# Kernel tuning notes

Measured on AMD Instinct MI355X. Metric: run time of the kernel, lower is better.

The kernel has to match this reference:

```python
import jax, jax.numpy as jnp
import numpy as np

# Dimensions (match input_specs / init_kwargs)
B, T, M, H, E, K = 4, 2048, 1024, 2048, 8, 2
CAP_FACTOR = 1.0  # tutel default capacity_factor
S = B * T
C = int(K * CAP_FACTOR * ((S + E - 1) // E))  # per-expert capacity (tutel Top-k gate)


def setup_inputs() -> dict:
    key = jax.random.key(0)
    ks = jax.random.split(key, 4)
    x = jax.random.normal(ks[0], (B, T, M), jnp.float32)
    wg = jax.random.normal(ks[1], (M, E), jnp.float32) / np.sqrt(M)
    w1 = jax.random.normal(ks[2], (E, M, H), jnp.float32) / np.sqrt(M)
    b1 = jnp.zeros((E, H), jnp.float32)
    w2 = jax.random.normal(ks[3], (E, H, M), jnp.float32) / np.sqrt(H)
    b2 = jnp.zeros((E, M), jnp.float32)
    return {"x": x, "wg": wg, "w1": w1, "b1": b1, "w2": w2, "b2": b2}


def reference(x, wg, w1, b1, w2, b2):
    xf = x.reshape(S, M)
    # ---- Top-k gate (fp32 gate) ----
    logits = xf.astype(jnp.float32) @ wg                 # [S, E]
    scores = jax.nn.softmax(logits, axis=-1)
    topv, topi = jax.lax.top_k(scores, K)                # [S, K]
    gates = topv / (jnp.sum(topv, axis=-1, keepdims=True) + 1e-9)  # normalized top-k gates

    # ---- Dispatch into [E, C, M] buffer with capacity-based token dropping ----
    buf = jnp.zeros((E, C, M), xf.dtype)
    offset = jnp.zeros((E,), jnp.int32)  # tokens already placed per expert (previous slots)
    pos_list, keep_list = [], []
    for j in range(K):  # small fixed loop over top-k slots
        e = topi[:, j]                                   # [S]
        m = jax.nn.one_hot(e, E, dtype=jnp.int32)        # [S, E]
        pos = jnp.sum(jnp.cumsum(m, axis=0) * m, axis=1) - 1 + offset[e]  # position within expert
        offset = offset + jnp.sum(m, axis=0)
        keep = pos < C                                   # drop tokens over capacity
        posc = jnp.minimum(pos, C - 1)
        buf = buf.at[e, posc].add(xf * keep[:, None].astype(xf.dtype))
        pos_list.append(posc)
        keep_list.append(keep)

    # ---- Grouped expert FFN: relu(x W1 + b1) W2 + b2 ----
    h = jax.nn.relu(jnp.einsum('ecm,emh->ech', buf, w1) + b1[:, None, :])  # [E, C, H]
    y = jnp.einsum('ech,ehm->ecm', h, w2) + b2[:, None, :]                 # [E, C, M]

    # ---- Combine with gate weights ----
    out = jnp.zeros_like(xf)
    for j in range(K):
        g = gates[:, j] * keep_list[j].astype(xf.dtype)
        out = out + g[:, None] * y[topi[:, j], pos_list[j]]

    out = out.reshape(B, T, M)
    # result = log_softmax(sum over model_dim, over token dim)
    return jax.nn.log_softmax(jnp.sum(out, axis=2), axis=1)   # [B, T]
```

## Files before the change

kernel.cpp:

```cpp
#include <hip/hip_runtime.h>
#include <hip/hip_bf16.h>
#include <cstdint>
#include <cstddef>

constexpr int Bb = 4;
constexpr int Tt = 2048;
constexpr int Mm = 1024;
constexpr int Hh = 2048;
constexpr int Ee = 8;
constexpr int Ss = Bb * Tt;
constexpr int Cc = 2048;

typedef __attribute__((ext_vector_type(4))) float f32x4;
typedef __attribute__((ext_vector_type(8))) short bf16x8;

__device__ inline void load_lds16(const void* g, void* l) {
    __builtin_amdgcn_global_load_lds(
        (const __attribute__((address_space(1))) unsigned int*)g,
        (__attribute__((address_space(3))) unsigned int*)l, 16, 0, 0);
}

__global__ __launch_bounds__(256) void k_prep(
    const float* __restrict__ w1, const float* __restrict__ w2, const float* __restrict__ b2,
    const float* __restrict__ x, const float* __restrict__ wg,
    __hip_bfloat16* __restrict__ w1t, float* __restrict__ w2sum, float* __restrict__ b2sum,
    int* __restrict__ esel, float* __restrict__ gates, __hip_bfloat16* __restrict__ xbf) {
    int bid = blockIdx.x;
    int t = threadIdx.x;
    if (bid < 4096) {
        __shared__ float tile[64][65];
        int e = bid >> 9, m0 = ((bid >> 5) & 15) * 64, h0 = (bid & 31) * 64;
        const float* src = w1 + (size_t)e * Mm * Hh;
        #pragma unroll
        for (int i = 0; i < 4; i++) {
            int idx = t + i * 256;
            int r = idx >> 4, c4 = idx & 15;
            float4 v = *(const float4*)(src + (size_t)(m0 + r) * Hh + h0 + c4 * 4);
            tile[r][c4 * 4 + 0] = v.x; tile[r][c4 * 4 + 1] = v.y;
            tile[r][c4 * 4 + 2] = v.z; tile[r][c4 * 4 + 3] = v.w;
        }
        __syncthreads();
        __hip_bfloat16* dst = w1t + (size_t)e * Hh * Mm;
        #pragma unroll
        for (int i = 0; i < 2; i++) {
            int idx = t + i * 256;
            int r = idx >> 3, c8 = idx & 7;
            __hip_bfloat16 tmp[8];
            #pragma unroll
            for (int k = 0; k < 8; k++) tmp[k] = __float2bfloat16(tile[c8 * 8 + k][r]);
            uint4 vv; __builtin_memcpy(&vv, tmp, 16);
            *(uint4*)(dst + (size_t)(h0 + r) * Mm + m0 + c8 * 8) = vv;
        }
    } else if (bid < 8192) {
        int wave = t >> 6, lane = t & 63;
        int r = (bid - 4096) * 4 + wave;
        const float4* p = (const float4*)(w2 + (size_t)r * Mm);
        float s = 0.f;
        #pragma unroll
        for (int i = 0; i < 4; i++) { float4 v = p[lane + i * 64]; s += v.x + v.y + v.z + v.w; }
        #pragma unroll
        for (int off = 32; off; off >>= 1) s += __shfl_down(s, off);
        if (lane == 0) w2sum[r] = s;
    } else if (bid == 8192) {
        int wave = t >> 6, lane = t & 63;
        int e = wave * 2 + (lane >> 5);
        int l = lane & 31;
        const float4* p = (const float4*)(b2 + (size_t)e * Mm);
        float s = 0.f;
        #pragma unroll
        for (int i = 0; i < 8; i++) { float4 v = p[l + i * 32]; s += v.x + v.y + v.z + v.w; }
        #pragma unroll
        for (int off = 16; off; off >>= 1) s += __shfl_down(s, off);
        if (l == 0) b2sum[e] = s;
    } else {
        int gb = bid - 8193;
        int s = (gb * 256 + t) >> 6;
        int lane = t & 63;
        const float4* xr = (const float4*)(x + (size_t)s * Mm);
        const float4* wgr = (const float4*)wg;
        float acc[8];
        #pragma unroll
        for (int e = 0; e < 8; e++) acc[e] = 0.f;
        #pragma unroll
        for (int i = 0; i < 4; i++) {
            float4 xv = xr[lane + i * 64];
            __hip_bfloat16 tb[4];
            tb[0] = __float2bfloat16(xv.x); tb[1] = __float2bfloat16(xv.y);
            tb[2] = __float2bfloat16(xv.z); tb[3] = __float2bfloat16(xv.w);
            uint2 u; __builtin_memcpy(&u, tb, 8);
            *(uint2*)(xbf + (size_t)s * Mm + (lane + i * 64) * 4) = u;
            int mbase = (lane + i * 64) * 4;
            #pragma unroll
            for (int k = 0; k < 4; k++) {
                int m = mbase + k;
                float xm = (k == 0) ? xv.x : (k == 1) ? xv.y : (k == 2) ? xv.z : xv.w;
                float4 w0 = wgr[m * 2], w1v = wgr[m * 2 + 1];
                acc[0] += xm * w0.x;  acc[1] += xm * w0.y;  acc[2] += xm * w0.z;  acc[3] += xm * w0.w;
                acc[4] += xm * w1v.x; acc[5] += xm * w1v.y; acc[6] += xm * w1v.z; acc[7] += xm * w1v.w;
            }
        }
        #pragma unroll
        for (int off = 32; off; off >>= 1)
            #pragma unroll
            for (int e = 0; e < 8; e++) acc[e] += __shfl_down(acc[e], off);
        if (lane == 0) {
            float mx = acc[0];
            #pragma unroll
            for (int e = 1; e < 8; e++) mx = fmaxf(mx, acc[e]);
            float p[8], se = 0.f;
            #pragma unroll
            for (int e = 0; e < 8; e++) { p[e] = expf(acc[e] - mx); se += p[e]; }
            float inv = 1.f / se;
            #pragma unroll
            for (int e = 0; e < 8; e++) p[e] *= inv;
            int i0 = 0; float v0 = p[0];
            #pragma unroll
            for (int e = 1; e < 8; e++) if (p[e] > v0) { v0 = p[e]; i0 = e; }
            int i1 = -1; float v1 = -1.f;
            #pragma unroll
            for (int e = 0; e < 8; e++) if (e != i0 && p[e] > v1) { v1 = p[e]; i1 = e; }
            float den = v0 + v1 + 1e-9f;
            esel[s] = i0; esel[Ss + s] = i1;
            gates[s] = v0 / den; gates[Ss + s] = v1 / den;
        }
    }
}

__global__ __launch_bounds__(256) void k_posA(const int* __restrict__ esel,
                                              int* __restrict__ lrank, int* __restrict__ blockhist) {
    int b = blockIdx.x, t = threadIdx.x;
    int d = b * 256 + t;
    int e = esel[d];
    int wave = t >> 6, lane = t & 63;
    __shared__ int wh[4][8];
    unsigned long long mymask = 0;
    #pragma unroll
    for (int q = 0; q < 8; q++) {
        unsigned long long m = __ballot(e == q);
        if (q == e) mymask = m;
        if (lane == 0) wh[wave][q] = (int)__popcll(m);
    }
    __syncthreads();
    int prefix = (int)__popcll(mymask & ((1ull << lane) - 1ull));
    for (int w = 0; w < wave; w++) prefix += wh[w][e];
    lrank[d] = prefix;
    if (t < 8) blockhist[b * 8 + t] = wh[0][t] + wh[1][t] + wh[2][t] + wh[3][t];
}

__global__ __launch_bounds__(512) void k_posB(const int* __restrict__ blockhist,
                                              int* __restrict__ blockbase) {
    int t = threadIdx.x;
    int wave = t >> 6, lane = t & 63;
    int v = blockhist[lane * 8 + wave];
    int x = v;
    #pragma unroll
    for (int off = 1; off < 64; off <<= 1) {
        int y = __shfl_up(x, off);
        if (lane >= off) x += y;
    }
    blockbase[lane * 8 + wave] = x - v;
}

__global__ __launch_bounds__(256) void k_sidx(const int* __restrict__ esel,
                                              const int* __restrict__ lrank,
                                              const int* __restrict__ blockbase,
                                              int* __restrict__ pos, int* __restrict__ srcidx) {
    int d = blockIdx.x * 256 + threadIdx.x;
    int e = esel[d];
    int p = blockbase[(d >> 8) * 8 + e] + lrank[d];
    pos[d] = p;
    if (p < Cc) srcidx[e * Cc + p] = d & (Ss - 1);
}

__global__ __launch_bounds__(256) void k_gemm(
    const __hip_bfloat16* __restrict__ xbf, const int* __restrict__ srcidx,
    const __hip_bfloat16* __restrict__ w1t,
    const float* __restrict__ b1, const float* __restrict__ w2sum,
    float* __restrict__ rowsum) {
    __shared__ __align__(16) __hip_bfloat16 As[2][128 * 32];
    __shared__ __align__(16) __hip_bfloat16 Bs[2][128 * 32];
    int bid = blockIdx.x;
    int e = bid & 7;
    int tile = bid >> 3;
    int sq = tile >> 4, in16 = tile & 15;
    int hb = (sq & 3) * 4 + (in16 & 3);
    int cb = (sq >> 2) * 4 + (in16 >> 2);
    int c0 = cb * 128, h0 = hb * 128;
    int t = threadIdx.x;
    int wave = t >> 6, lane = t & 63;
    int wm = wave >> 1, wn = wave & 1;
    int r16 = lane & 15, quad = lane >> 4;
    int r_s = t >> 2;
    int qd = ((t & 3) - ((t >> 3) & 3)) & 3;
    int s0 = srcidx[e * Cc + c0 + r_s];
    int s1 = srcidx[e * Cc + c0 + 64 + r_s];
    const __hip_bfloat16* a0 = xbf + (size_t)s0 * Mm + qd * 8;
    const __hip_bfloat16* a1 = xbf + (size_t)s1 * Mm + qd * 8;
    const __hip_bfloat16* Bp = w1t + (size_t)e * Hh * Mm;
    const __hip_bfloat16* b0 = Bp + (size_t)(h0 + r_s) * Mm + qd * 8;
    const __hip_bfloat16* b1p = Bp + (size_t)(h0 + 64 + r_s) * Mm + qd * 8;
    int frag = r16 * 4 + ((quad + (r16 >> 1)) & 3);
    f32x4 acc[4][4];
    #pragma unroll
    for (int i = 0; i < 4; i++)
        #pragma unroll
        for (int j = 0; j < 4; j++) acc[i][j] = (f32x4){0.f, 0.f, 0.f, 0.f};

    load_lds16(a0,  As[0] + t * 8);
    load_lds16(a1,  As[0] + (256 + t) * 8);
    load_lds16(b0,  Bs[0] + t * 8);
    load_lds16(b1p, Bs[0] + (256 + t) * 8);

    #pragma unroll 2
    for (int tt = 0; tt < 32; ++tt) {
        int cur = tt & 1;
        __builtin_amdgcn_sched_barrier(0);
        if (tt < 31) {
            int k0 = (tt + 1) * 32;
            load_lds16(a0 + k0,  As[cur ^ 1] + t * 8);
            load_lds16(a1 + k0,  As[cur ^ 1] + (256 + t) * 8);
            load_lds16(b0 + k0,  Bs[cur ^ 1] + t * 8);
            load_lds16(b1p + k0, Bs[cur ^ 1] + (256 + t) * 8);
            asm volatile("s_waitcnt vmcnt(4)" ::: "memory");
        } else {
            asm volatile("s_waitcnt vmcnt(0)" ::: "memory");
        }
        __builtin_amdgcn_s_barrier();
        __builtin_amdgcn_sched_barrier(0);
        bf16x8 af[4], bfr[4];
        #pragma unroll
        for (int mi = 0; mi < 4; mi++)
            af[mi] = *(const bf16x8*)(As[cur] + (((wm * 4 + mi) * 64 + frag) * 8));
        #pragma unroll
        for (int ni = 0; ni < 4; ni++)
            bfr[ni] = *(const bf16x8*)(Bs[cur] + (((wn * 4 + ni) * 64 + frag) * 8));
        #pragma unroll
        for (int mi = 0; mi < 4; mi++)
            #pragma unroll
            for (int ni = 0; ni < 4; ni++)
                acc[mi][ni] = __builtin_amdgcn_mfma_f32_16x16x32_bf16(af[mi], bfr[ni], acc[mi][ni], 0, 0, 0);
        __builtin_amdgcn_sched_barrier(0);
        __builtin_amdgcn_s_barrier();
    }

    float b1v[4], wsv[4];
    #pragma unroll
    for (int ni = 0; ni < 4; ni++) {
        int hg = h0 + wn * 64 + ni * 16 + r16;
        b1v[ni] = b1[e * Hh + hg];
        wsv[ni] = w2sum[e * Hh + hg];
    }
    #pragma unroll
    for (int mi = 0; mi < 4; mi++) {
        #pragma unroll
        for (int r = 0; r < 4; r++) {
            float val = 0.f;
            #pragma unroll
            for (int ni = 0; ni < 4; ni++) {
                float sv = acc[mi][ni][r] + b1v[ni];
                val += fmaxf(sv, 0.f) * wsv[ni];
            }
            #pragma unroll
            for (int off = 1; off < 16; off <<= 1) val += __shfl_xor(val, off);
            if (r16 == 0) {
                int cg = c0 + wm * 64 + mi * 16 + quad * 4 + r;
                atomicAdd(&rowsum[e * Cc + cg], val);
            }
        }
    }
}

__global__ __launch_bounds__(256) void k_combine(
    const int* __restrict__ esel, const int* __restrict__ pos,
    const float* __restrict__ gates, const float* __restrict__ rowsum,
    const float* __restrict__ b2sum, float* __restrict__ vals) {
    int s = blockIdx.x * 256 + threadIdx.x;
    float acc = 0.f;
    #pragma unroll
    for (int j = 0; j < 2; j++) {
        int d = j * Ss + s;
        int p = pos[d];
        if (p < Cc) {
            int ee = esel[d];
            acc += gates[d] * (rowsum[ee * Cc + p] + b2sum[ee]);
        }
    }
    vals[s] = acc;
}

__global__ __launch_bounds__(1024) void k_lsm(const float* __restrict__ vals,
                                              float* __restrict__ out) {
    int b = blockIdx.x; int t = threadIdx.x;
    __shared__ float red[1024];
    float v0 = vals[b * Tt + t];
    float v1 = vals[b * Tt + t + 1024];
    float m = fmaxf(v0, v1);
    red[t] = m; __syncthreads();
    for (int st = 512; st; st >>= 1) { if (t < st) red[t] = fmaxf(red[t], red[t + st]); __syncthreads(); }
    float mx = red[0];
    __syncthreads();
    float se = expf(v0 - mx) + expf(v1 - mx);
    red[t] = se; __syncthreads();
    for (int st = 512; st; st >>= 1) { if (t < st) red[t] += red[t + st]; __syncthreads(); }
    float lse = logf(red[0]);
    out[b * Tt + t] = v0 - mx - lse;
    out[b * Tt + t + 1024] = v1 - mx - lse;
}

extern "C" void kernel_launch(void* const* d_in, const int* in_sizes, int n_in,
                              void* d_out, int out_size, void* d_ws, size_t ws_size,
                              hipStream_t stream) {
    const float* x  = (const float*)d_in[0];
    const float* wg = (const float*)d_in[1];
    const float* w1 = (const float*)d_in[2];
    const float* b1 = (const float*)d_in[3];
    const float* w2 = (const float*)d_in[4];
    const float* b2 = (const float*)d_in[5];
    float* out = (float*)d_out;

    char* ws = (char*)d_ws;
    size_t off = 0;
    auto alloc = [&](size_t bytes) -> void* {
        void* p = ws + off;
        off += (bytes + 255) & ~(size_t)255;
        return p;
    };
    float* rowsum   = (float*)alloc((size_t)Ee * Cc * 4 + (size_t)Ee * Cc * 4);
    int*   srcidx   = (int*)(rowsum + (size_t)Ee * Cc);
    float* w2sum    = (float*)alloc((size_t)Ee * Hh * 4);
    float* b2sum    = (float*)alloc(Ee * 4);
    int*   esel     = (int*)alloc((size_t)2 * Ss * 4);
    int*   lrank    = (int*)alloc((size_t)2 * Ss * 4);
    int*   blockhist= (int*)alloc((size_t)64 * 8 * 4);
    int*   blockbase= (int*)alloc((size_t)64 * 8 * 4);
    int*   pos      = (int*)alloc((size_t)2 * Ss * 4);
    float* gates    = (float*)alloc((size_t)2 * Ss * 4);
    __hip_bfloat16* xbf = (__hip_bfloat16*)alloc((size_t)Ss * Mm * 2);
    __hip_bfloat16* w1t = (__hip_bfloat16*)alloc((size_t)Ee * Hh * Mm * 2);

    hipMemsetAsync(rowsum, 0, (size_t)2 * Ee * Cc * 4, stream);
    k_prep<<<10241, 256, 0, stream>>>(w1, w2, b2, x, wg, w1t, w2sum, b2sum, esel, gates, xbf);
    k_posA<<<64, 256, 0, stream>>>(esel, lrank, blockhist);
    k_posB<<<1, 512, 0, stream>>>(blockhist, blockbase);
    k_sidx<<<64, 256, 0, stream>>>(esel, lrank, blockbase, pos, srcidx);
    k_gemm<<<2048, 256, 0, stream>>>(xbf, srcidx, w1t, b1, w2sum, rowsum);
    float* vals = (float*)lrank;
    k_combine<<<32, 256, 0, stream>>>(esel, pos, gates, rowsum, b2sum, vals);
    k_lsm<<<Bb, 1024, 0, stream>>>(vals, out);
}
```

Before: 308.5 us.

## Enlarge expert GEMM tiles to 256x256 with 8 waves and 4-stage LDS pipeline

```diff
diff --git a/kernel.cpp b/kernel.cpp
--- a/kernel.cpp
+++ b/kernel.cpp
@@ -172,76 +172,102 @@
     if (p < Cc) srcidx[e * Cc + p] = d & (Ss - 1);
 }
 
-__global__ __launch_bounds__(256) void k_gemm(
+__global__ __launch_bounds__(512, 2) void k_gemm(
     const __hip_bfloat16* __restrict__ xbf, const int* __restrict__ srcidx,
     const __hip_bfloat16* __restrict__ w1t,
     const float* __restrict__ b1, const float* __restrict__ w2sum,
     float* __restrict__ rowsum) {
-    __shared__ __align__(16) __hip_bfloat16 As[2][128 * 32];
-    __shared__ __align__(16) __hip_bfloat16 Bs[2][128 * 32];
+    __shared__ __align__(16) __hip_bfloat16 As[4][256 * 32];
+    __shared__ __align__(16) __hip_bfloat16 Bs[4][256 * 32];
     int bid = blockIdx.x;
     int e = bid & 7;
     int tile = bid >> 3;
-    int sq = tile >> 4, in16 = tile & 15;
-    int hb = (sq & 3) * 4 + (in16 & 3);
-    int cb = (sq >> 2) * 4 + (in16 >> 2);
-    int c0 = cb * 128, h0 = hb * 128;
+    int cb = tile >> 3, hb = tile & 7;
+    int c0 = cb * 256, h0 = hb * 256;
     int t = threadIdx.x;
     int wave = t >> 6, lane = t & 63;
-    int wm = wave >> 1, wn = wave & 1;
+    int wm = wave >> 2;
+    int wn = wave & 3;
     int r16 = lane & 15, quad = lane >> 4;
     int r_s = t >> 2;
     int qd = ((t & 3) - ((t >> 3) & 3)) & 3;
     int s0 = srcidx[e * Cc + c0 + r_s];
-    int s1 = srcidx[e * Cc + c0 + 64 + r_s];
+    int s1 = srcidx[e * Cc + c0 + 128 + r_s];
     const __hip_bfloat16* a0 = xbf + (size_t)s0 * Mm + qd * 8;
     const __hip_bfloat16* a1 = xbf + (size_t)s1 * Mm + qd * 8;
     const __hip_bfloat16* Bp = w1t + (size_t)e * Hh * Mm;
     const __hip_bfloat16* b0 = Bp + (size_t)(h0 + r_s) * Mm + qd * 8;
-    const __hip_bfloat16* b1p = Bp + (size_t)(h0 + 64 + r_s) * Mm + qd * 8;
-    int frag = r16 * 4 + ((quad + (r16 >> 1)) & 3);
-    f32x4 acc[4][4];
-    #pragma unroll
-    for (int i = 0; i < 4; i++)
+    const __hip_bfloat16* b1p = Bp + (size_t)(h0 + 128 + r_s) * Mm + qd * 8;
+    int fo = r16 * 4 + ((quad + (r16 >> 1)) & 3);
+    f32x4 acc[8][4];
+    #pragma unroll
+    for (int i = 0; i < 8; i++)
         #pragma unroll
         for (int j = 0; j < 4; j++) acc[i][j] = (f32x4){0.f, 0.f, 0.f, 0.f};
 
-    load_lds16(a0,  As[0] + t * 8);
-    load_lds16(a1,  As[0] + (256 + t) * 8);
-    load_lds16(b0,  Bs[0] + t * 8);
-    load_lds16(b1p, Bs[0] + (256 + t) * 8);
-
-    #pragma unroll 2
-    for (int tt = 0; tt < 32; ++tt) {
-        int cur = tt & 1;
+    #pragma unroll
+    for (int p = 0; p < 3; p++) {
+        int k0 = p * 32;
+        load_lds16(a0 + k0,  As[p] + t * 8);
+        load_lds16(a1 + k0,  As[p] + (512 + t) * 8);
+        load_lds16(b0 + k0,  Bs[p] + t * 8);
+        load_lds16(b1p + k0, Bs[p] + (512 + t) * 8);
+    }
+
+    for (int j = 0; j < 29; ++j) {
         __builtin_amdgcn_sched_barrier(0);
-        if (tt < 31) {
-            int k0 = (tt + 1) * 32;
-            load_lds16(a0 + k0,  As[cur ^ 1] + t * 8);
-            load_lds16(a1 + k0,  As[cur ^ 1] + (256 + t) * 8);
-            load_lds16(b0 + k0,  Bs[cur ^ 1] + t * 8);
-            load_lds16(b1p + k0, Bs[cur ^ 1] + (256 + t) * 8);
-            asm volatile("s_waitcnt vmcnt(4)" ::: "memory");
-        } else {
-            asm volatile("s_waitcnt vmcnt(0)" ::: "memory");
-        }
+        asm volatile("s_waitcnt vmcnt(8)" ::: "memory");
         __builtin_amdgcn_s_barrier();
         __builtin_amdgcn_sched_barrier(0);
-        bf16x8 af[4], bfr[4];
-        #pragma unroll
-        for (int mi = 0; mi < 4; mi++)
-            af[mi] = *(const bf16x8*)(As[cur] + (((wm * 4 + mi) * 64 + frag) * 8));
+        {
+            int b = (j + 3) & 3;
+            int k0 = (j + 3) * 32;
+            load_lds16(a0 + k0,  As[b] + t * 8);
+            load_lds16(a1 + k0,  As[b] + (512 + t) * 8);
+            load_lds16(b0 + k0,  Bs[b] + t * 8);
+            load_lds16(b1p + k0, Bs[b] + (512 + t) * 8);
+        }
+        const __hip_bfloat16* Ar = As[j & 3];
+        const __hip_bfloat16* Br = Bs[j & 3];
+        bf16x8 bfr[4];
         #pragma unroll
         for (int ni = 0; ni < 4; ni++)
-            bfr[ni] = *(const bf16x8*)(Bs[cur] + (((wn * 4 + ni) * 64 + frag) * 8));
-        #pragma unroll
-        for (int mi = 0; mi < 4; mi++)
+            bfr[ni] = *(const bf16x8*)(Br + ((wn * 4 + ni) * 64 + fo) * 8);
+        __builtin_amdgcn_s_setprio(1);
+        #pragma unroll
+        for (int mi = 0; mi < 8; mi++) {
+            bf16x8 af = *(const bf16x8*)(Ar + ((wm * 8 + mi) * 64 + fo) * 8);
             #pragma unroll
             for (int ni = 0; ni < 4; ni++)
-                acc[mi][ni] = __builtin_amdgcn_mfma_f32_16x16x32_bf16(af[mi], bfr[ni], acc[mi][ni], 0, 0, 0);
+                acc[mi][ni] = __builtin_amdgcn_mfma_f32_16x16x32_bf16(af, bfr[ni], acc[mi][ni], 0, 0, 0);
+        }
+        __builtin_amdgcn_s_setprio(0);
+    }
+    #pragma unroll
+    for (int j = 29; j < 32; ++j) {
         __builtin_amdgcn_sched_barrier(0);
+        if (j == 29)      asm volatile("s_waitcnt vmcnt(8)" ::: "memory");
+        else if (j == 30) asm volatile("s_waitcnt vmcnt(4)" ::: "memory");
+        else              asm volatile("s_waitcnt vmcnt(0)" ::: "memory");
         __builtin_amdgcn_s_barrier();
-    }
+        __builtin_amdgcn_sched_barrier(0);
+        const __hip_bfloat16* Ar = As[j & 3];
+        const __hip_bfloat16* Br = Bs[j & 3];
+        bf16x8 bfr[4];
+        #pragma unroll
+        for (int ni = 0; ni < 4; ni++)
+            bfr[ni] = *(const bf16x8*)(Br + ((wn * 4 + ni) * 64 + fo) * 8);
+        __builtin_amdgcn_s_setprio(1);
+        #pragma unroll
+        for (int mi = 0; mi < 8; mi++) {
+            bf16x8 af = *(const bf16x8*)(Ar + ((wm * 8 + mi) * 64 + fo) * 8);
+            #pragma unroll
+            for (int ni = 0; ni < 4; ni++)
+                acc[mi][ni] = __builtin_amdgcn_mfma_f32_16x16x32_bf16(af, bfr[ni], acc[mi][ni], 0, 0, 0);
+        }
+        __builtin_amdgcn_s_setprio(0);
+    }
+    __builtin_amdgcn_sched_barrier(0);
 
     float b1v[4], wsv[4];
     #pragma unroll
@@ -251,7 +277,7 @@
         wsv[ni] = w2sum[e * Hh + hg];
     }
     #pragma unroll
-    for (int mi = 0; mi < 4; mi++) {
+    for (int mi = 0; mi < 8; mi++) {
         #pragma unroll
         for (int r = 0; r < 4; r++) {
             float val = 0.f;
@@ -263,7 +289,7 @@
             #pragma unroll
             for (int off = 1; off < 16; off <<= 1) val += __shfl_xor(val, off);
             if (r16 == 0) {
-                int cg = c0 + wm * 64 + mi * 16 + quad * 4 + r;
+                int cg = c0 + wm * 128 + mi * 16 + quad * 4 + r;
                 atomicAdd(&rowsum[e * Cc + cg], val);
             }
         }
@@ -343,7 +369,7 @@
     k_posA<<<64, 256, 0, stream>>>(esel, lrank, blockhist);
     k_posB<<<1, 512, 0, stream>>>(blockhist, blockbase);
     k_sidx<<<64, 256, 0, stream>>>(esel, lrank, blockbase, pos, srcidx);
-    k_gemm<<<2048, 256, 0, stream>>>(xbf, srcidx, w1t, b1, w2sum, rowsum);
+    k_gemm<<<512, 512, 0, stream>>>(xbf, srcidx, w1t, b1, w2sum, rowsum);
     float* vals = (float*)lrank;
     k_combine<<<32, 256, 0, stream>>>(esel, pos, gates, rowsum, b2sum, vals);
     k_lsm<<<Bb, 1024, 0, stream>>>(vals, out);
```

Result: no change. 307.1 us (-0.4%).
